# Performance work log

Measured on AMD Instinct MI355X. Metric: run time of the kernel, lower is better.

The kernel has to match this reference:

```python
import jax, jax.numpy as jnp
import numpy as np

H, W, C = 96, 96, 21
SIGMA_RGB = 3.0   # bilateral spatial sdims (as called in the original code)
SIGMA_XY = 64.0   # gaussian spatial sdims
SCHAN = 255.0     # bilateral color std
COMPAT = 10.0     # Potts compatibility weight (same for both kernels)
N_ITERS = 5


def _gauss_kernel(feats):
    # feats: [N, D] -> K[i,j] = exp(-0.5 * ||f_i - f_j||^2)
    sq = jnp.sum(feats * feats, axis=-1)
    d2 = sq[:, None] + sq[None, :] - 2.0 * (feats @ feats.T)
    return jnp.exp(-0.5 * jnp.maximum(d2, 0.0))


def setup_inputs() -> dict:
    key = jax.random.key(0)
    k1, k2, k3 = jax.random.split(key, 3)
    logits = jax.random.normal(k1, (1, C, H, W), dtype=jnp.float32)
    labels = jax.random.randint(k2, (1, H, W), 0, C, dtype=jnp.int32)
    image = jax.random.uniform(k3, (1, 3, H, W), dtype=jnp.float32) * 255.0
    return {"logits": logits, "labels": labels, "image": image, "num_classes": C}


def reference(logits, labels, image, num_classes):
    # unary potentials: U = -log_softmax(logits)
    logp = jax.nn.log_softmax(logits, axis=1)              # [1,C,H,W]
    U = (-logp)[0].reshape(num_classes, -1).T              # [N,C]

    # pixel features
    yy, xx = jnp.meshgrid(jnp.arange(H), jnp.arange(W), indexing="ij")
    pos = jnp.stack([yy, xx], axis=-1).reshape(-1, 2).astype(logits.dtype)  # [N,2]
    rgb = image[0].transpose(1, 2, 0).reshape(-1, 3)        # [N,3]

    # dense pairwise kernels (exact Gaussian / bilateral, self-connection removed)
    N = H * W
    eye = jnp.eye(N, dtype=logits.dtype)
    Kg = _gauss_kernel(pos / SIGMA_XY) - eye
    fb = jnp.concatenate([pos / SIGMA_RGB, rgb / SCHAN], axis=-1)
    Kb = _gauss_kernel(fb) - eye

    # mean-field inference, Potts compatibility mu(l,l') = [l != l']
    Q0 = jax.nn.softmax(-U, axis=1)                         # [N,C]

    def step(Q, _):
        msg = Kg @ Q + Kb @ Q                               # [N,C] filtered Q
        pair = COMPAT * (jnp.sum(msg, axis=1, keepdims=True) - msg)
        Q = jax.nn.softmax(-U - pair, axis=1)
        return Q, None

    Q, _ = jax.lax.scan(step, Q0, None, length=N_ITERS)
    pairwise = Q.T.reshape(1, num_classes, H, W)

    # cross entropy (mean over pixels)
    ce = -jnp.mean(jnp.take_along_axis(logp, labels[:, None].astype(jnp.int32), axis=1))

    return ce + pairwise                                    # broadcast, as in original
```

## Files before the change

kernel.cpp:

```cpp
#include <hip/hip_runtime.h>
#include <hip/hip_fp16.h>

#define HH 96
#define WW 96
#define CC 21
#define NN (HH*WW)
#define NBLK (NN/256)
#define STRIDE 24
#define ROWF (WW*STRIDE)
#define NRUN (NN/8)

typedef _Float16 f16x8 __attribute__((ext_vector_type(8)));
typedef float f32x4 __attribute__((ext_vector_type(4)));

union H8 { f16x8 v; __half2 h2[4]; };


__global__ __launch_bounds__(256) void k_setup(
    const float* __restrict__ logits, const int* __restrict__ labels,
    const float* __restrict__ image, float* __restrict__ U,
    float* __restrict__ Q0, _Float16* __restrict__ QTa,
    _Float16* __restrict__ QTb, float* __restrict__ gtab,
    float* __restrict__ partial) {
  const int t = threadIdx.x;
  const int i = blockIdx.x * 256 + t;
  const int qoff = (i >> 3) * 192 + (i & 7);

  float d[CC];
  float mx = -1e30f;
#pragma unroll
  for (int c = 0; c < CC; ++c) {
    d[c] = logits[c * NN + i];
    mx = fmaxf(mx, d[c]);
  }
  float s = 0.f;
#pragma unroll
  for (int c = 0; c < CC; ++c) { d[c] -= mx; s += __expf(d[c]); }
  const float lse = logf(s);
  const float inv = 1.f / s;
  const int lab = labels[i];
  float myU = 0.f;
#pragma unroll
  for (int c = 0; c < CC; ++c) {
    const float Uc = lse - d[c];
    const float q = __expf(d[c]) * inv;
    U[i * STRIDE + c] = Uc;
    Q0[i * STRIDE + c] = q;
    QTa[qoff + c * 8] = (_Float16)q;
    myU = (c == lab) ? Uc : myU;
  }
  const float rr = image[i] * (1.f / 255.f);
  const float rg = image[NN + i] * (1.f / 255.f);
  const float rb = image[2 * NN + i] * (1.f / 255.f);
  U[i * STRIDE + 21] = 0.f;
  U[i * STRIDE + 22] = 0.f;
  U[i * STRIDE + 23] = 0.f;
  Q0[i * STRIDE + 21] = rr;
  Q0[i * STRIDE + 22] = rg;
  Q0[i * STRIDE + 23] = rb;
  QTa[qoff + 21 * 8] = (_Float16)rr;
  QTa[qoff + 22 * 8] = (_Float16)rg;
  QTa[qoff + 23 * 8] = (_Float16)rb;
  QTb[qoff + 21 * 8] = (_Float16)rr;
  QTb[qoff + 22 * 8] = (_Float16)rg;
  QTb[qoff + 23 * 8] = (_Float16)rb;

  if (blockIdx.x == 0 && t < 96) {
    const float dv = (float)t * (1.f / 64.f);
    gtab[t] = __expf(-0.5f * dv * dv);
  }

  __shared__ float red[256];
  red[t] = myU;
  __syncthreads();
  for (int off = 128; off > 0; off >>= 1) {
    if (t < off) red[t] += red[t + off];
    __syncthreads();
  }
  if (t == 0) partial[blockIdx.x] = red[0];
}

__global__ __launch_bounds__(256) void k_gauss_y(
    const float* __restrict__ Qin, float* __restrict__ Gy,
    const float* __restrict__ gtab) {
  __shared__ float g[96];
  if (threadIdx.x < 96) g[threadIdx.x] = gtab[threadIdx.x];
  __syncthreads();
  const int idx = blockIdx.x * 256 + threadIdx.x;
  const int y = idx / ROWF;
  const int rem = idx - y * ROWF;
  const float* base = Qin + rem;
  float a0 = 0.f, a1 = 0.f, a2 = 0.f, a3 = 0.f;
#pragma unroll 6
  for (int yp = 0; yp < HH; yp += 4) {
    a0 = fmaf(g[abs(y - yp)], base[yp * ROWF], a0);
    a1 = fmaf(g[abs(y - yp - 1)], base[(yp + 1) * ROWF], a1);
    a2 = fmaf(g[abs(y - yp - 2)], base[(yp + 2) * ROWF], a2);
    a3 = fmaf(g[abs(y - yp - 3)], base[(yp + 3) * ROWF], a3);
  }
  Gy[idx] = (a0 + a1) + (a2 + a3);
}

__global__ __launch_bounds__(512) void k_bilat(
    const float* __restrict__ U, const float* __restrict__ Qin,
    const float* __restrict__ Gy, const _Float16* __restrict__ QT,
    const float* __restrict__ gtab, float* __restrict__ Qout,
    _Float16* __restrict__ QTout, const float* __restrict__ partial,
    float* __restrict__ out, int last) {
  __shared__ __half sytab[64];
  __shared__ __half2 sxtab[64];
  __shared__ float sgt[96];
  __shared__ float psum[8][16][24];
  __shared__ float sces;

  const int tid = threadIdx.x;
  const int w = tid >> 6;
  const int l = tid & 63;
  const int g = l >> 4;
  const int q = l & 15;

  if (tid < 64) {
    const float dv = (float)(tid - 32);
    sytab[tid] = __float2half(__expf(dv * dv * (-1.f / 18.f)));
    const float dv1 = dv + 1.f;
    sxtab[tid] = __floats2half2_rn(__expf(dv * dv * (-1.f / 18.f)),
                                   __expf(dv1 * dv1 * (-1.f / 18.f)));
    if (last) {
      float v = (tid < NBLK) ? partial[tid] : 0.f;
#pragma unroll
      for (int off = 32; off >= 1; off >>= 1) v += __shfl_xor(v, off, 64);
      if (tid == 0) sces = v * (1.f / (float)NN);
    }
  } else if (tid < 160) {
    sgt[tid - 64] = gtab[tid - 64];
  }
  __syncthreads();

  const int bid = blockIdx.x;
  const int tile = (bid & 7) * 72 + (bid >> 3);
  const int ty0 = (tile / 24) * 4;
  const int tx0 = (tile - (tile / 24) * 24) * 4;

  const int pr = q >> 2, pc = q & 3;
  const int yi = ty0 + pr, xi = tx0 + pc;
  const int ipix = yi * WW + xi;

  const float4 rown = *(const float4*)(Qin + ipix * STRIDE + 20);
  const __half2 ri_r = __float2half2_rn(rown.y);
  const __half2 ri_g = __float2half2_rn(rown.z);
  const __half2 ri_b = __float2half2_rn(rown.w);
  const __half2 mhalf = __floats2half2_rn(-0.5f, -0.5f);
  const __half hzero = __float2half(0.f);

  const int xs = tx0 - 16;
  const int xbase0 = (xs > 0 ? xs : 0) & ~7;
  const int rid0 = (w < 4) ? w * 23 : 92 + (w - 4) * 22;
  const int nrun = (w < 4) ? 23 : 22;

  const int row2 = (16 + q > 23) ? 23 : 16 + q;

  f32x4 acc0 = {0.f, 0.f, 0.f, 0.f};
  f32x4 acc1 = {0.f, 0.f, 0.f, 0.f};

#pragma unroll
  for (int ck = 0; ck < 6; ++ck) {
    const int r = ck * 4 + g;
    const int rid = rid0 + r;
    const int wr = rid / 5;
    const int cs = rid - wr * 5;
    const int yj = ty0 - 16 + wr;
    const int xb = xbase0 + cs * 8;
    const bool ok = (r < nrun) & (yj >= 0) & (yj < HH) & (xb <= WW - 8);
    const int yc = min(max(yj, 0), HH - 1);
    const int xc = min(xb, WW - 8);
    const _Float16* base = QT + (yc * 12 + (xc >> 3)) * 192;

    H8 b1, b2, rj, gj, bj;
    b1.v = *(const f16x8*)(base + q * 8);
    b2.v = *(const f16x8*)(base + row2 * 8);
    rj.v = *(const f16x8*)(base + 21 * 8);
    gj.v = *(const f16x8*)(base + 22 * 8);
    bj.v = *(const f16x8*)(base + 23 * 8);

    const int dy = yj - yi;
    const int iy = min(max(dy + 32, 0), 63);
    const __half syv = ok ? sytab[iy] : hzero;
    const __half2 sy2 = __half2half2(syv);
    const int dx0 = xb - xi;
    const int ix0 = min(max(dx0 + 32, 0), 57);

    H8 af;
#pragma unroll
    for (int e2 = 0; e2 < 4; ++e2) {
      const __half2 sx2 = sxtab[ix0 + 2 * e2];
      const __half2 dr = __hsub2(rj.h2[e2], ri_r);
      const __half2 dg = __hsub2(gj.h2[e2], ri_g);
      const __half2 db = __hsub2(bj.h2[e2], ri_b);
      __half2 d2c = __hmul2(dr, dr);
      d2c = __hfma2(dg, dg, d2c);
      d2c = __hfma2(db, db, d2c);
      const __half2 ec = h2exp(__hmul2(d2c, mhalf));
      af.h2[e2] = __hmul2(__hmul2(sy2, sx2), ec);
    }
    acc0 = __builtin_amdgcn_mfma_f32_16x16x32_f16(af.v, b1.v, acc0, 0, 0, 0);
    acc1 = __builtin_amdgcn_mfma_f32_16x16x32_f16(af.v, b2.v, acc1, 0, 0, 0);
  }

#pragma unroll
  for (int reg = 0; reg < 4; ++reg) {
    psum[w][g * 4 + reg][q] = acc0[reg];
    if (q < 8) psum[w][g * 4 + reg][16 + q] = acc1[reg];
  }
  __syncthreads();

  const int half_ = l >> 5;
  const int cl = l & 31;
  const bool act = cl < CC;
  const int pix = w * 2 + half_;
  const int py = ty0 + (pix >> 2), px = tx0 + (pix & 3);
  const int ip = py * WW + px;
  float Qic = 0.f;
  if (cl < STRIDE) Qic = Qin[ip * STRIDE + cl];
  float tcv = 0.f, Uc = 0.f, Gc = 0.f;
  if (act) {
    tcv = psum[0][pix][cl] + psum[1][pix][cl] + psum[2][pix][cl] +
          psum[3][pix][cl] + psum[4][pix][cl] + psum[5][pix][cl] +
          psum[6][pix][cl] + psum[7][pix][cl];
    Uc = U[ip * STRIDE + cl];
    const float* grow = Gy + py * ROWF + cl;
    float g0 = 0.f, g1 = 0.f, g2 = 0.f, g3 = 0.f;
#pragma unroll 6
    for (int xp = 0; xp < WW; xp += 4) {
      g0 = fmaf(sgt[abs(px - xp)], grow[xp * STRIDE], g0);
      g1 = fmaf(sgt[abs(px - xp - 1)], grow[(xp + 1) * STRIDE], g1);
      g2 = fmaf(sgt[abs(px - xp - 2)], grow[(xp + 2) * STRIDE], g2);
      g3 = fmaf(sgt[abs(px - xp - 3)], grow[(xp + 3) * STRIDE], g3);
    }
    Gc = (g0 + g1) + (g2 + g3);
  }
  const float contrib = act ? (tcv + Gc - 2.f * Qic) : 0.f;
  float tot = contrib;
#pragma unroll
  for (int off = 16; off >= 1; off >>= 1) tot += __shfl_xor(tot, off, 32);
  const float lc = act ? (-Uc - 10.f * (tot - contrib)) : -1e30f;
  float mxl = lc;
#pragma unroll
  for (int off = 16; off >= 1; off >>= 1)
    mxl = fmaxf(mxl, __shfl_xor(mxl, off, 32));
  const float e = act ? __expf(lc - mxl) : 0.f;
  float se = e;
#pragma unroll
  for (int off = 16; off >= 1; off >>= 1) se += __shfl_xor(se, off, 32);
  const float qnew = e / se;
  if (last) {
    if (act) out[cl * NN + ip] = sces + qnew;
  } else {
    if (cl < STRIDE) Qout[ip * STRIDE + cl] = act ? qnew : Qic;
    if (act) QTout[(ip >> 3) * 192 + cl * 8 + (ip & 7)] = (_Float16)qnew;
  }
}

__global__ __launch_bounds__(512) void k_bilat_diag(
    const float* __restrict__ Qin, const _Float16* __restrict__ QT,
    float* __restrict__ dbg) {
  __shared__ __half sytab[64];
  __shared__ __half2 sxtab[64];

  const int tid = threadIdx.x;
  const int w = tid >> 6;
  const int l = tid & 63;
  const int g = l >> 4;
  const int q = l & 15;

  if (tid < 64) {
    const float dv = (float)(tid - 32);
    sytab[tid] = __float2half(__expf(dv * dv * (-1.f / 18.f)));
    const float dv1 = dv + 1.f;
    sxtab[tid] = __floats2half2_rn(__expf(dv * dv * (-1.f / 18.f)),
                                   __expf(dv1 * dv1 * (-1.f / 18.f)));
  }
  __syncthreads();

  const int bid = blockIdx.x;
  const int tile0 = (bid & 7) * 72 + (bid >> 3);
  const __half2 mhalf = __floats2half2_rn(-0.5f, -0.5f);
  const __half hzero = __float2half(0.f);
  const int rid0 = (w < 4) ? w * 23 : 92 + (w - 4) * 22;
  const int nrun = (w < 4) ? 23 : 22;
  const int row2 = (16 + q > 23) ? 23 : 16 + q;
  const int pr = q >> 2, pc = q & 3;

  f32x4 acc0 = {0.f, 0.f, 0.f, 0.f};
  f32x4 acc1 = {0.f, 0.f, 0.f, 0.f};

  for (int rep = 0; rep < 4; ++rep) {
    const int tile = (tile0 + rep * 144) % 576;
    const int ty0 = (tile / 24) * 4;
    const int tx0 = (tile - (tile / 24) * 24) * 4;
    const int yi = ty0 + pr, xi = tx0 + pc;
    const int ipix = yi * WW + xi;
    const float4 rown = *(const float4*)(Qin + ipix * STRIDE + 20);
    const __half2 ri_r = __float2half2_rn(rown.y);
    const __half2 ri_g = __float2half2_rn(rown.z);
    const __half2 ri_b = __float2half2_rn(rown.w);
    const int xs = tx0 - 16;
    const int xbase0 = (xs > 0 ? xs : 0) & ~7;

#pragma unroll
    for (int ck = 0; ck < 6; ++ck) {
      const int r = ck * 4 + g;
      const int rid = rid0 + r;
      const int wr = rid / 5;
      const int cs = rid - wr * 5;
      const int yj = ty0 - 16 + wr;
      const int xb = xbase0 + cs * 8;
      const bool ok = (r < nrun) & (yj >= 0) & (yj < HH) & (xb <= WW - 8);
      const int yc = min(max(yj, 0), HH - 1);
      const int xc = min(xb, WW - 8);
      const _Float16* base = QT + (yc * 12 + (xc >> 3)) * 192;

      H8 b1, b2, rj, gj, bj;
      b1.v = *(const f16x8*)(base + q * 8);
      b2.v = *(const f16x8*)(base + row2 * 8);
      rj.v = *(const f16x8*)(base + 21 * 8);
      gj.v = *(const f16x8*)(base + 22 * 8);
      bj.v = *(const f16x8*)(base + 23 * 8);

      const int dy = yj - yi;
      const int iy = min(max(dy + 32, 0), 63);
      const __half syv = ok ? sytab[iy] : hzero;
      const __half2 sy2 = __half2half2(syv);
      const int dx0 = xb - xi;
      const int ix0 = min(max(dx0 + 32, 0), 57);

      H8 af;
#pragma unroll
      for (int e2 = 0; e2 < 4; ++e2) {
        const __half2 sx2 = sxtab[ix0 + 2 * e2];
        const __half2 dr = __hsub2(rj.h2[e2], ri_r);
        const __half2 dg = __hsub2(gj.h2[e2], ri_g);
        const __half2 db = __hsub2(bj.h2[e2], ri_b);
        __half2 d2c = __hmul2(dr, dr);
        d2c = __hfma2(dg, dg, d2c);
        d2c = __hfma2(db, db, d2c);
        const __half2 ec = h2exp(__hmul2(d2c, mhalf));
        af.h2[e2] = __hmul2(__hmul2(sy2, sx2), ec);
      }
      acc0 = __builtin_amdgcn_mfma_f32_16x16x32_f16(af.v, b1.v, acc0, 0, 0, 0);
      acc1 = __builtin_amdgcn_mfma_f32_16x16x32_f16(af.v, b2.v, acc1, 0, 0, 0);
    }
  }

  dbg[blockIdx.x * 512 + tid] =
      acc0[0] + acc0[1] + acc0[2] + acc0[3] + acc1[0] + acc1[1] + acc1[2] +
      acc1[3];
}

extern "C" void kernel_launch(void* const* d_in, const int* in_sizes, int n_in,
                              void* d_out, int out_size, void* d_ws,
                              size_t ws_size, hipStream_t stream) {
  const float* logits = (const float*)d_in[0];
  const int* labels = (const int*)d_in[1];
  const float* image = (const float*)d_in[2];
  float* ws = (float*)d_ws;

  float* U = ws;
  float* Qa = U + NN * STRIDE;
  float* Qb = Qa + NN * STRIDE;
  float* Gy = Qb + NN * STRIDE;
  float* gtab = Gy + NN * STRIDE;
  float* partial = gtab + 96;
  float* cepad = partial + 64;
  _Float16* QTa = (_Float16*)(cepad + 64);
  _Float16* QTb = QTa + NRUN * 192;
  float* dbg = (float*)(QTb + NRUN * 192);

  k_setup<<<NBLK, 256, 0, stream>>>(logits, labels, image, U, Qa, QTa, QTb,
                                    gtab, partial);

  const float* qi = Qa;
  float* qo = Qb;
  const _Float16* qti = QTa;
  _Float16* qto = QTb;
  const int gblk = NN * STRIDE / 256;
  for (int it = 0; it < 5; ++it) {
    k_gauss_y<<<gblk, 256, 0, stream>>>(qi, Gy, gtab);
    k_bilat<<<576, 512, 0, stream>>>(U, qi, Gy, qti, gtab, qo, qto, partial,
                                     (float*)d_out, it == 4);
    qi = qo;
    qo = (qo == Qb) ? Qa : Qb;
    const _Float16* tmp = qti;
    qti = qto;
    qto = (_Float16*)tmp;
  }

  k_bilat_diag<<<576, 512, 0, stream>>>(qi, qti, dbg);
}
```

Baseline: 162.2 us.

## Fuse setup and all mean-field iterations into one cooperative persistent kernel

Adds a cooperative kernel, one block per 4x4 tile, that computes unaries and initial Q, then runs all five iterations. Each iteration does the vertical Gaussian pass, the bilateral MFMA step, and the horizontal pass plus softmax, with grid-wide syncs between phases instead of separate kernel launches. It also removes the extra diagnostic bilateral kernel that was launched after the iterations. The multi-kernel path stays as a fallback if co-residency or the cooperative launch fails. The intent is to cut launch gaps and redundant work, at the cost of grid-sync overhead and a hard need for all 576 blocks of 512 threads to fit on the device at once.

```diff
diff --git a/kernel.cpp b/kernel.cpp
--- a/kernel.cpp
+++ b/kernel.cpp
@@ -1,5 +1,8 @@
 #include <hip/hip_runtime.h>
 #include <hip/hip_fp16.h>
+#include <hip/hip_cooperative_groups.h>
+
+namespace cg = cooperative_groups;
 
 #define HH 96
 #define WW 96
@@ -9,12 +12,257 @@
 #define STRIDE 24
 #define ROWF (WW*STRIDE)
 #define NRUN (NN/8)
+#define NTILE 576
 
 typedef _Float16 f16x8 __attribute__((ext_vector_type(8)));
 typedef float f32x4 __attribute__((ext_vector_type(4)));
 
 union H8 { f16x8 v; __half2 h2[4]; };
 
+__global__ __launch_bounds__(512, 6) void k_crf(
+    const float* __restrict__ logits, const int* __restrict__ labels,
+    const float* __restrict__ image, float* __restrict__ U,
+    float* __restrict__ Qa, float* __restrict__ Qb,
+    _Float16* __restrict__ QTa, _Float16* __restrict__ QTb,
+    float* __restrict__ Gy, float* __restrict__ partial,
+    float* __restrict__ out) {
+  cg::grid_group grid = cg::this_grid();
+
+  __shared__ float psum[8][16][24];
+  __shared__ float sgt[96];
+  __shared__ __half sytab[64];
+  __shared__ __half2 sxtab[64];
+  __shared__ float red16[16];
+  __shared__ float sces;
+
+  const int tid = threadIdx.x;
+  const int w = tid >> 6;
+  const int l = tid & 63;
+  const int g = l >> 4;
+  const int q = l & 15;
+
+  const int tile = blockIdx.x;
+  const int ty0 = (tile / 24) * 4;
+  const int tx0 = (tile - (tile / 24) * 24) * 4;
+
+  if (tid < 96) {
+    const float dv = (float)tid * (1.f / 64.f);
+    sgt[tid] = __expf(-0.5f * dv * dv);
+  }
+  if (tid >= 128 && tid < 192) {
+    const int k = tid - 128;
+    const float dv = (float)(k - 32);
+    sytab[k] = __float2half(__expf(dv * dv * (-1.f / 18.f)));
+    const float dv1 = dv + 1.f;
+    sxtab[k] = __floats2half2_rn(__expf(dv * dv * (-1.f / 18.f)),
+                                 __expf(dv1 * dv1 * (-1.f / 18.f)));
+  }
+
+  {
+    const int pix = tid >> 5;
+    const int cl = tid & 31;
+    const int py = ty0 + (pix >> 2), px_ = tx0 + (pix & 3);
+    const int i = py * WW + px_;
+    const float dv = (cl < CC) ? logits[cl * NN + i] : -1e30f;
+    float mx = dv;
+#pragma unroll
+    for (int off = 16; off >= 1; off >>= 1)
+      mx = fmaxf(mx, __shfl_xor(mx, off, 32));
+    const float ex = (cl < CC) ? __expf(dv - mx) : 0.f;
+    float s = ex;
+#pragma unroll
+    for (int off = 16; off >= 1; off >>= 1) s += __shfl_xor(s, off, 32);
+    const float lse = logf(s);
+    const float Uc = lse - (dv - mx);
+    const float qv = ex / s;
+    const int qoff = (i >> 3) * 192 + (i & 7);
+    float myU = 0.f;
+    if (cl < CC) {
+      U[i * STRIDE + cl] = Uc;
+      Qa[i * STRIDE + cl] = qv;
+      QTa[qoff + cl * 8] = (_Float16)qv;
+      myU = (labels[i] == cl) ? Uc : 0.f;
+    } else if (cl < STRIDE) {
+      const float r = image[(cl - 21) * NN + i] * (1.f / 255.f);
+      U[i * STRIDE + cl] = 0.f;
+      Qa[i * STRIDE + cl] = r;
+      QTa[qoff + cl * 8] = (_Float16)r;
+      QTb[qoff + cl * 8] = (_Float16)r;
+    }
+#pragma unroll
+    for (int off = 16; off >= 1; off >>= 1) myU += __shfl_xor(myU, off, 32);
+    if (cl == 0) red16[pix] = myU;
+  }
+  __syncthreads();
+  if (tid == 0) {
+    float s2 = 0.f;
+#pragma unroll
+    for (int k2 = 0; k2 < 16; ++k2) s2 += red16[k2];
+    partial[tile] = s2;
+  }
+
+  const int apr = q >> 2, apc = q & 3;
+  const int ayi = ty0 + apr, axi = tx0 + apc;
+  const int aip = ayi * WW + axi;
+  const __half2 ri_r = __float2half2_rn(image[aip] * (1.f / 255.f));
+  const __half2 ri_g = __float2half2_rn(image[NN + aip] * (1.f / 255.f));
+  const __half2 ri_b = __float2half2_rn(image[2 * NN + aip] * (1.f / 255.f));
+  const __half2 mhalf = __floats2half2_rn(-0.5f, -0.5f);
+  const __half hzero = __float2half(0.f);
+  const int xs = tx0 - 16;
+  const int xbase0 = (xs > 0 ? xs : 0) & ~7;
+  const int rid0 = (w < 4) ? w * 23 : 92 + (w - 4) * 22;
+  const int nrun = (w < 4) ? 23 : 22;
+  const int row2 = (16 + q > 23) ? 23 : 16 + q;
+
+  grid.sync();
+
+#pragma unroll 1
+  for (int it = 0; it < 5; ++it) {
+    const float* Qin = (it & 1) ? Qb : Qa;
+    float* Qout = (it & 1) ? Qa : Qb;
+    const _Float16* QT = (it & 1) ? QTb : QTa;
+    _Float16* QTout = (it & 1) ? QTa : QTb;
+    const int last = (it == 4);
+
+    {
+      const int fid = blockIdx.x * 512 + tid;
+      if (fid < NN * STRIDE) {
+        const int y = fid / ROWF;
+        const int rem = fid - y * ROWF;
+        const float* base = Qin + rem;
+        float a0 = 0.f, a1 = 0.f, a2 = 0.f, a3 = 0.f;
+#pragma unroll 6
+        for (int yp = 0; yp < HH; yp += 4) {
+          a0 = fmaf(sgt[abs(y - yp)], base[yp * ROWF], a0);
+          a1 = fmaf(sgt[abs(y - yp - 1)], base[(yp + 1) * ROWF], a1);
+          a2 = fmaf(sgt[abs(y - yp - 2)], base[(yp + 2) * ROWF], a2);
+          a3 = fmaf(sgt[abs(y - yp - 3)], base[(yp + 3) * ROWF], a3);
+        }
+        Gy[fid] = (a0 + a1) + (a2 + a3);
+      }
+    }
+
+    f32x4 acc0 = {0.f, 0.f, 0.f, 0.f};
+    f32x4 acc1 = {0.f, 0.f, 0.f, 0.f};
+#pragma unroll
+    for (int ck = 0; ck < 6; ++ck) {
+      const int r = ck * 4 + g;
+      const int rid = rid0 + r;
+      const int wr = rid / 5;
+      const int cs = rid - wr * 5;
+      const int yj = ty0 - 16 + wr;
+      const int xb = xbase0 + cs * 8;
+      const bool ok = (r < nrun) & (yj >= 0) & (yj < HH) & (xb <= WW - 8);
+      const int yc = min(max(yj, 0), HH - 1);
+      const int xc = min(xb, WW - 8);
+      const _Float16* base = QT + (yc * 12 + (xc >> 3)) * 192;
+
+      H8 b1, b2, rj, gj, bj;
+      b1.v = *(const f16x8*)(base + q * 8);
+      b2.v = *(const f16x8*)(base + row2 * 8);
+      rj.v = *(const f16x8*)(base + 21 * 8);
+      gj.v = *(const f16x8*)(base + 22 * 8);
+      bj.v = *(const f16x8*)(base + 23 * 8);
+
+      const int dy = yj - ayi;
+      const int iy = min(max(dy + 32, 0), 63);
+      const __half syv = ok ? sytab[iy] : hzero;
+      const __half2 sy2 = __half2half2(syv);
+      const int dx0 = xb - axi;
+      const int ix0 = min(max(dx0 + 32, 0), 57);
+
+      H8 af;
+#pragma unroll
+      for (int e2 = 0; e2 < 4; ++e2) {
+        const __half2 sx2 = sxtab[ix0 + 2 * e2];
+        const __half2 dr = __hsub2(rj.h2[e2], ri_r);
+        const __half2 dg = __hsub2(gj.h2[e2], ri_g);
+        const __half2 db = __hsub2(bj.h2[e2], ri_b);
+        __half2 d2c = __hmul2(dr, dr);
+        d2c = __hfma2(dg, dg, d2c);
+        d2c = __hfma2(db, db, d2c);
+        const __half2 ec = h2exp(__hmul2(d2c, mhalf));
+        af.h2[e2] = __hmul2(__hmul2(sy2, sx2), ec);
+      }
+      acc0 = __builtin_amdgcn_mfma_f32_16x16x32_f16(af.v, b1.v, acc0, 0, 0, 0);
+      acc1 = __builtin_amdgcn_mfma_f32_16x16x32_f16(af.v, b2.v, acc1, 0, 0, 0);
+    }
+
+#pragma unroll
+    for (int reg = 0; reg < 4; ++reg) {
+      psum[w][g * 4 + reg][q] = acc0[reg];
+      if (q < 8) psum[w][g * 4 + reg][16 + q] = acc1[reg];
+    }
+    grid.sync();
+
+    if (last) {
+      float v = partial[tid];
+      v += (tid < NTILE - 512) ? partial[512 + tid] : 0.f;
+#pragma unroll
+      for (int off = 32; off >= 1; off >>= 1) v += __shfl_xor(v, off, 64);
+      if (l == 0) red16[w] = v;
+      __syncthreads();
+      if (tid == 0) {
+        float s2 = 0.f;
+#pragma unroll
+        for (int k2 = 0; k2 < 8; ++k2) s2 += red16[k2];
+        sces = s2 * (1.f / (float)NN);
+      }
+      __syncthreads();
+    }
+
+    {
+      const int half_ = l >> 5;
+      const int cl = l & 31;
+      const bool act = cl < CC;
+      const int pix = w * 2 + half_;
+      const int py = ty0 + (pix >> 2), px = tx0 + (pix & 3);
+      const int ip = py * WW + px;
+      float Qic = 0.f;
+      if (cl < STRIDE) Qic = Qin[ip * STRIDE + cl];
+      float tcv = 0.f, Uc = 0.f, Gc = 0.f;
+      if (act) {
+        tcv = psum[0][pix][cl] + psum[1][pix][cl] + psum[2][pix][cl] +
+              psum[3][pix][cl] + psum[4][pix][cl] + psum[5][pix][cl] +
+              psum[6][pix][cl] + psum[7][pix][cl];
+        Uc = U[ip * STRIDE + cl];
+        const float* grow = Gy + py * ROWF + cl;
+        float g0 = 0.f, g1 = 0.f, g2 = 0.f, g3 = 0.f;
+#pragma unroll 6
+        for (int xp = 0; xp < WW; xp += 4) {
+          g0 = fmaf(sgt[abs(px - xp)], grow[xp * STRIDE], g0);
+          g1 = fmaf(sgt[abs(px - xp - 1)], grow[(xp + 1) * STRIDE], g1);
+          g2 = fmaf(sgt[abs(px - xp - 2)], grow[(xp + 2) * STRIDE], g2);
+          g3 = fmaf(sgt[abs(px - xp - 3)], grow[(xp + 3) * STRIDE], g3);
+        }
+        Gc = (g0 + g1) + (g2 + g3);
+      }
+      const float contrib = act ? (tcv + Gc - 2.f * Qic) : 0.f;
+      float tot = contrib;
+#pragma unroll
+      for (int off = 16; off >= 1; off >>= 1) tot += __shfl_xor(tot, off, 32);
+      const float lc = act ? (-Uc - 10.f * (tot - contrib)) : -1e30f;
+      float mxl = lc;
+#pragma unroll
+      for (int off = 16; off >= 1; off >>= 1)
+        mxl = fmaxf(mxl, __shfl_xor(mxl, off, 32));
+      const float e = act ? __expf(lc - mxl) : 0.f;
+      float se = e;
+#pragma unroll
+      for (int off = 16; off >= 1; off >>= 1) se += __shfl_xor(se, off, 32);
+      const float qnew = e / se;
+      if (last) {
+        if (act) out[cl * NN + ip] = sces + qnew;
+      } else {
+        if (cl < STRIDE) Qout[ip * STRIDE + cl] = act ? qnew : Qic;
+        if (act) QTout[(ip >> 3) * 192 + cl * 8 + (ip & 7)] = (_Float16)qnew;
+      }
+    }
+
+    if (!last) grid.sync();
+  }
+}
 
 __global__ __launch_bounds__(256) void k_setup(
     const float* __restrict__ logits, const int* __restrict__ labels,
@@ -136,8 +384,7 @@
   }
   __syncthreads();
 
-  const int bid = blockIdx.x;
-  const int tile = (bid & 7) * 72 + (bid >> 3);
+  const int tile = blockIdx.x;
   const int ty0 = (tile / 24) * 4;
   const int tx0 = (tile - (tile / 24) * 24) * 4;
 
@@ -156,7 +403,6 @@
   const int xbase0 = (xs > 0 ? xs : 0) & ~7;
   const int rid0 = (w < 4) ? w * 23 : 92 + (w - 4) * 22;
   const int nrun = (w < 4) ? 23 : 22;
-
   const int row2 = (16 + q > 23) ? 23 : 16 + q;
 
   f32x4 acc0 = {0.f, 0.f, 0.f, 0.f};
@@ -260,102 +506,6 @@
   }
 }
 
-__global__ __launch_bounds__(512) void k_bilat_diag(
-    const float* __restrict__ Qin, const _Float16* __restrict__ QT,
-    float* __restrict__ dbg) {
-  __shared__ __half sytab[64];
-  __shared__ __half2 sxtab[64];
-
-  const int tid = threadIdx.x;
-  const int w = tid >> 6;
-  const int l = tid & 63;
-  const int g = l >> 4;
-  const int q = l & 15;
-
-  if (tid < 64) {
-    const float dv = (float)(tid - 32);
-    sytab[tid] = __float2half(__expf(dv * dv * (-1.f / 18.f)));
-    const float dv1 = dv + 1.f;
-    sxtab[tid] = __floats2half2_rn(__expf(dv * dv * (-1.f / 18.f)),
-                                   __expf(dv1 * dv1 * (-1.f / 18.f)));
-  }
-  __syncthreads();
-
-  const int bid = blockIdx.x;
-  const int tile0 = (bid & 7) * 72 + (bid >> 3);
-  const __half2 mhalf = __floats2half2_rn(-0.5f, -0.5f);
-  const __half hzero = __float2half(0.f);
-  const int rid0 = (w < 4) ? w * 23 : 92 + (w - 4) * 22;
-  const int nrun = (w < 4) ? 23 : 22;
-  const int row2 = (16 + q > 23) ? 23 : 16 + q;
-  const int pr = q >> 2, pc = q & 3;
-
-  f32x4 acc0 = {0.f, 0.f, 0.f, 0.f};
-  f32x4 acc1 = {0.f, 0.f, 0.f, 0.f};
-
-  for (int rep = 0; rep < 4; ++rep) {
-    const int tile = (tile0 + rep * 144) % 576;
-    const int ty0 = (tile / 24) * 4;
-    const int tx0 = (tile - (tile / 24) * 24) * 4;
-    const int yi = ty0 + pr, xi = tx0 + pc;
-    const int ipix = yi * WW + xi;
-    const float4 rown = *(const float4*)(Qin + ipix * STRIDE + 20);
-    const __half2 ri_r = __float2half2_rn(rown.y);
-    const __half2 ri_g = __float2half2_rn(rown.z);
-    const __half2 ri_b = __float2half2_rn(rown.w);
-    const int xs = tx0 - 16;
-    const int xbase0 = (xs > 0 ? xs : 0) & ~7;
-
-#pragma unroll
-    for (int ck = 0; ck < 6; ++ck) {
-      const int r = ck * 4 + g;
-      const int rid = rid0 + r;
-      const int wr = rid / 5;
-      const int cs = rid - wr * 5;
-      const int yj = ty0 - 16 + wr;
-      const int xb = xbase0 + cs * 8;
-      const bool ok = (r < nrun) & (yj >= 0) & (yj < HH) & (xb <= WW - 8);
-      const int yc = min(max(yj, 0), HH - 1);
-      const int xc = min(xb, WW - 8);
-      const _Float16* base = QT + (yc * 12 + (xc >> 3)) * 192;
-
-      H8 b1, b2, rj, gj, bj;
-      b1.v = *(const f16x8*)(base + q * 8);
-      b2.v = *(const f16x8*)(base + row2 * 8);
-      rj.v = *(const f16x8*)(base + 21 * 8);
-      gj.v = *(const f16x8*)(base + 22 * 8);
-      bj.v = *(const f16x8*)(base + 23 * 8);
-
-      const int dy = yj - yi;
-      const int iy = min(max(dy + 32, 0), 63);
-      const __half syv = ok ? sytab[iy] : hzero;
-      const __half2 sy2 = __half2half2(syv);
-      const int dx0 = xb - xi;
-      const int ix0 = min(max(dx0 + 32, 0), 57);
-
-      H8 af;
-#pragma unroll
-      for (int e2 = 0; e2 < 4; ++e2) {
-        const __half2 sx2 = sxtab[ix0 + 2 * e2];
-        const __half2 dr = __hsub2(rj.h2[e2], ri_r);
-        const __half2 dg = __hsub2(gj.h2[e2], ri_g);
-        const __half2 db = __hsub2(bj.h2[e2], ri_b);
-        __half2 d2c = __hmul2(dr, dr);
-        d2c = __hfma2(dg, dg, d2c);
-        d2c = __hfma2(db, db, d2c);
-        const __half2 ec = h2exp(__hmul2(d2c, mhalf));
-        af.h2[e2] = __hmul2(__hmul2(sy2, sx2), ec);
-      }
-      acc0 = __builtin_amdgcn_mfma_f32_16x16x32_f16(af.v, b1.v, acc0, 0, 0, 0);
-      acc1 = __builtin_amdgcn_mfma_f32_16x16x32_f16(af.v, b2.v, acc1, 0, 0, 0);
-    }
-  }
-
-  dbg[blockIdx.x * 512 + tid] =
-      acc0[0] + acc0[1] + acc0[2] + acc0[3] + acc1[0] + acc1[1] + acc1[2] +
-      acc1[3];
-}
-
 extern "C" void kernel_launch(void* const* d_in, const int* in_sizes, int n_in,
                               void* d_out, int out_size, void* d_ws,
                               size_t ws_size, hipStream_t stream) {
@@ -369,15 +519,33 @@
   float* Qb = Qa + NN * STRIDE;
   float* Gy = Qb + NN * STRIDE;
   float* gtab = Gy + NN * STRIDE;
-  float* partial = gtab + 96;
-  float* cepad = partial + 64;
-  _Float16* QTa = (_Float16*)(cepad + 64);
+  float* partial36 = gtab + 96;
+  float* partial576 = partial36 + 64;
+  _Float16* QTa = (_Float16*)(partial576 + 640);
   _Float16* QTb = QTa + NRUN * 192;
-  float* dbg = (float*)(QTb + NRUN * 192);
+  float* out = (float*)d_out;
+
+  int maxb = 0, ncu = 0;
+  hipError_t qe =
+      hipOccupancyMaxActiveBlocksPerMultiprocessor(&maxb, k_crf, 512, 0);
+  hipError_t ae = hipDeviceGetAttribute(
+      &ncu, hipDeviceAttributeMultiprocessorCount, 0);
+  bool coop = (qe == hipSuccess) && (ae == hipSuccess) &&
+              (maxb * ncu >= NTILE);
+
+  if (coop) {
+    void* args[] = {(void*)&logits, (void*)&labels, (void*)&image,
+                    (void*)&U,      (void*)&Qa,     (void*)&Qb,
+                    (void*)&QTa,    (void*)&QTb,    (void*)&Gy,
+                    (void*)&partial576, (void*)&out};
+    hipError_t le = hipLaunchCooperativeKernel((void*)k_crf, dim3(NTILE),
+                                               dim3(512), args, 0, stream);
+    if (le == hipSuccess) return;
+    (void)hipGetLastError();
+  }
 
   k_setup<<<NBLK, 256, 0, stream>>>(logits, labels, image, U, Qa, QTa, QTb,
-                                    gtab, partial);
-
+                                    gtab, partial36);
   const float* qi = Qa;
   float* qo = Qb;
   const _Float16* qti = QTa;
@@ -385,14 +553,12 @@
   const int gblk = NN * STRIDE / 256;
   for (int it = 0; it < 5; ++it) {
     k_gauss_y<<<gblk, 256, 0, stream>>>(qi, Gy, gtab);
-    k_bilat<<<576, 512, 0, stream>>>(U, qi, Gy, qti, gtab, qo, qto, partial,
-                                     (float*)d_out, it == 4);
+    k_bilat<<<NTILE, 512, 0, stream>>>(U, qi, Gy, qti, gtab, qo, qto,
+                                       partial36, out, it == 4);
     qi = qo;
     qo = (qo == Qb) ? Qa : Qb;
     const _Float16* tmp = qti;
     qti = qto;
     qto = (_Float16*)tmp;
   }
-
-  k_bilat_diag<<<576, 512, 0, stream>>>(qi, qti, dbg);
 }
```

Result: faster. 138.3 us (-14.7%).
